# Performance work log

Hardware: AMD Instinct MI355X
Metric: run time of the kernel (lower is better)

## Reference

```python
import jax, jax.numpy as jnp
from jax import lax
import numpy as np

VOCAB, TAGS, EMB, HID = 50000, 45, 256, 512
B, S = 32, 256


def setup_inputs() -> dict:
    key = jax.random.key(0)
    ks = jax.random.split(key, 12)
    sc = 0.05
    return {
        "x": jax.random.randint(ks[0], (B, S), 0, VOCAB),
        "tags": jax.random.randint(ks[1], (B, S), 0, TAGS),
        "emb": jax.random.normal(ks[2], (VOCAB, EMB), jnp.float32) * sc,
        "w_ih_f": jax.random.normal(ks[3], (4 * HID, EMB), jnp.float32) * sc,
        "w_hh_f": jax.random.normal(ks[4], (4 * HID, HID), jnp.float32) * sc,
        "b_f": jnp.zeros((4 * HID,), jnp.float32),
        "w_ih_b": jax.random.normal(ks[5], (4 * HID, EMB), jnp.float32) * sc,
        "w_hh_b": jax.random.normal(ks[6], (4 * HID, HID), jnp.float32) * sc,
        "b_b": jnp.zeros((4 * HID,), jnp.float32),
        "lin_w": jax.random.normal(ks[7], (TAGS, 2 * HID), jnp.float32) * sc,
        "lin_b": jnp.zeros((TAGS,), jnp.float32),
        "start_t": jax.random.normal(ks[8], (TAGS,), jnp.float32) * 0.1,
        "end_t": jax.random.normal(ks[9], (TAGS,), jnp.float32) * 0.1,
        "trans": jax.random.normal(ks[10], (TAGS,), jnp.float32)[:, None] * 0.0 + jax.random.normal(ks[11], (TAGS, TAGS), jnp.float32) * 0.1,
    }


def _lstm_dir(xs, w_ih, w_hh, b, reverse):
    # xs: [B,S,E]. PyTorch gate order: i, f, g, o.
    Bsz = xs.shape[0]
    H = w_hh.shape[1]
    def step(carry, x_t):
        h, c = carry
        g = x_t @ w_ih.T + h @ w_hh.T + b
        i, f, gg, o = jnp.split(g, 4, axis=-1)
        c = jax.nn.sigmoid(f) * c + jax.nn.sigmoid(i) * jnp.tanh(gg)
        h = jax.nn.sigmoid(o) * jnp.tanh(c)
        return (h, c), h
    init = (jnp.zeros((Bsz, H), xs.dtype), jnp.zeros((Bsz, H), xs.dtype))
    _, hs = lax.scan(step, init, jnp.swapaxes(xs, 0, 1), reverse=reverse)
    return jnp.swapaxes(hs, 0, 1)  # [B,S,H]


def _crf_nll(em, tags, start_t, end_t, trans):
    # em: [B,S,T]; numerator: score of gold path
    em_sc = jnp.take_along_axis(em, tags[..., None], axis=2)[..., 0].sum(axis=1)
    tr_sc = trans[tags[:, :-1], tags[:, 1:]].sum(axis=1)
    score = start_t[tags[:, 0]] + em_sc + tr_sc + end_t[tags[:, -1]]
    # partition function via forward algorithm (logsumexp recurrence)
    alpha0 = start_t + em[:, 0]  # [B,T]
    def step(alpha, e_t):
        alpha = jax.nn.logsumexp(alpha[:, :, None] + trans[None], axis=1) + e_t
        return alpha, None
    alpha, _ = lax.scan(step, alpha0, jnp.swapaxes(em[:, 1:], 0, 1))
    logZ = jax.nn.logsumexp(alpha + end_t, axis=1)
    return -(score - logZ).mean()  # reduction='mean', loss = -llh


def reference(x, tags, emb, w_ih_f, w_hh_f, b_f, w_ih_b, w_hh_b, b_b,
              lin_w, lin_b, start_t, end_t, trans):
    embeds = emb[x]                               # [B,S,E]
    h_f = _lstm_dir(embeds, w_ih_f, w_hh_f, b_f, False)
    h_b = _lstm_dir(embeds, w_ih_b, w_hh_b, b_b, True)
    lstm_out = jnp.concatenate([h_f, h_b], axis=-1)  # [B,S,2H]
    emissions = lstm_out @ lin_w.T + lin_b           # [B,S,T]
    return _crf_nll(emissions, tags, start_t, end_t, trans)
```

## Files before the change

kernel.cpp:

```cpp
#include <hip/hip_runtime.h>

#define BB 32
#define SS 256
#define EMBD 256
#define HIDD 512
#define NTAG 45
#define TPAD 48
#define NBLK 32
#define APAD 520
#define GRID_REC 64
#define SENT 0x01010101u

typedef __bf16 bf16x8 __attribute__((ext_vector_type(8)));
typedef float  f32x4  __attribute__((ext_vector_type(4)));
typedef short  s16x8  __attribute__((ext_vector_type(8)));
typedef unsigned u32x4 __attribute__((ext_vector_type(4)));

__device__ __forceinline__ unsigned short f2bf(float x) {
  unsigned u = __builtin_bit_cast(unsigned, x);
  u = (u + 0x7fffu + ((u >> 16) & 1u)) >> 16;
  return (unsigned short)u;
}
__device__ __forceinline__ float bf2f(unsigned short u) {
  unsigned v = ((unsigned)u) << 16; return __builtin_bit_cast(float, v);
}

__device__ __forceinline__ void st32_sys(unsigned* p, unsigned v) {
  asm volatile("global_store_dword %0, %1, off sc0 sc1" :: "v"(p), "v"(v) : "memory");
}

#define LD8(CPOL)                                                           \
  asm volatile("global_load_dwordx4 %0, %[q0], off " CPOL "\n\t"            \
               "global_load_dwordx4 %1, %[q1], off " CPOL "\n\t"            \
               "global_load_dwordx4 %2, %[q2], off " CPOL "\n\t"            \
               "global_load_dwordx4 %3, %[q3], off " CPOL "\n\t"            \
               "global_load_dwordx4 %4, %[q4], off " CPOL "\n\t"            \
               "global_load_dwordx4 %5, %[q5], off " CPOL "\n\t"            \
               "global_load_dwordx4 %6, %[q6], off " CPOL "\n\t"            \
               "global_load_dwordx4 %7, %[q7], off " CPOL "\n\t"            \
               "s_waitcnt vmcnt(0)"                                         \
               : "=&v"(v0), "=&v"(v1), "=&v"(v2), "=&v"(v3),                \
                 "=&v"(v4), "=&v"(v5), "=&v"(v6), "=&v"(v7)                 \
               : [q0] "v"(p), [q1] "v"(p + 2048), [q2] "v"(p + 4096),       \
                 [q3] "v"(p + 6144), [q4] "v"(p + 8192), [q5] "v"(p + 10240),\
                 [q6] "v"(p + 12288), [q7] "v"(p + 14336)                   \
               : "memory")

__global__ void k_pack_e(const int* __restrict__ x, const float* __restrict__ emb,
                         unsigned short* __restrict__ E) {
  int idx = blockIdx.x * 256 + threadIdx.x;
  int e = idx & 255; int bt = idx >> 8; int b = bt & 31; int t = bt >> 5;
  int tok = x[b * SS + t];
  E[idx] = f2bf(emb[(long)tok * EMBD + e]);
}

__global__ void k_pack_w(const float* __restrict__ wih_f, const float* __restrict__ whh_f,
                         const float* __restrict__ bf_,  const float* __restrict__ wih_b,
                         const float* __restrict__ whh_b, const float* __restrict__ bb_,
                         unsigned short* __restrict__ Wh, unsigned short* __restrict__ Wie,
                         float* __restrict__ Bh) {
  long idx = (long)blockIdx.x * 256 + threadIdx.x;
  int k = (int)(idx % 768); long rest = idx / 768;
  int r2 = (int)(rest & 2047); int dir = (int)(rest >> 11);
  int blk = r2 >> 6, rl = r2 & 63, gate = rl >> 4, hl = rl & 15;
  int orig = gate * HIDD + blk * 16 + hl;
  const float* wih = dir ? wih_b : wih_f;
  const float* whh = dir ? whh_b : whh_f;
  if (k < HIDD) Wh[((long)(dir * 2048 + r2)) * 512 + k] = f2bf(whh[(long)orig * HIDD + k]);
  else          Wie[((long)(dir * 2048 + r2)) * 256 + (k - 512)] = f2bf(wih[(long)orig * EMBD + (k - 512)]);
  if (k == 0) {
    const float* bias = dir ? bb_ : bf_;
    Bh[dir * 2048 + r2] = bias[orig];
  }
}

__global__ void k_pack_l(const float* __restrict__ lin_w, const float* __restrict__ lin_b,
                         unsigned short* __restrict__ LW, float* __restrict__ LB) {
  int idx = blockIdx.x * 256 + threadIdx.x;
  if (idx < TPAD * 1024) {
    int tag = idx >> 10; int c = idx & 1023;
    LW[idx] = (tag < NTAG) ? f2bf(lin_w[tag * 1024 + c]) : (unsigned short)0;
  } else if (idx < TPAD * 1024 + TPAD) {
    int tag = idx - TPAD * 1024;
    LB[tag] = (tag < NTAG) ? lin_b[tag] : 0.f;
  }
}

__launch_bounds__(256)
__global__ void k_eproj(const unsigned short* __restrict__ E,
                        const unsigned short* __restrict__ Wie,
                        const float* __restrict__ Bh,
                        unsigned short* __restrict__ Ep) {
  __shared__ unsigned short W2[64 * 264];
  const int bx = blockIdx.x;
  const int tg = bx & 63, blk = (bx >> 6) & 31, dir = bx >> 11;
  const int tid = threadIdx.x;
  const int w = tid >> 6, lane = tid & 63;
  const int lm = lane & 15, quad = lane >> 4;

  {
    const unsigned short* src = Wie + ((long)(dir * 2048 + blk * 64)) * 256;
    for (int i = 0; i < 8; ++i) {
      int c = i * 256 + tid;
      int row = c >> 5, off = c & 31;
      *(s16x8*)&W2[row * 264 + off * 8] = *(const s16x8*)&src[row * 256 + off * 8];
    }
  }
  __syncthreads();

  f32x4 acc[2][4] = {};
#pragma unroll
  for (int kk = 0; kk < 8; ++kk) {
    s16x8 av[2];
#pragma unroll
    for (int sub = 0; sub < 2; ++sub)
      av[sub] = *(const s16x8*)&E[((long)(tg * 128 + w * 32 + sub * 16 + lm)) * 256 + kk * 32 + quad * 8];
#pragma unroll
    for (int sub = 0; sub < 2; ++sub)
#pragma unroll
      for (int n = 0; n < 4; ++n) {
        s16x8 bs = *(const s16x8*)&W2[(n * 16 + lm) * 264 + kk * 32 + quad * 8];
        acc[sub][n] = __builtin_amdgcn_mfma_f32_16x16x32_bf16(
            __builtin_bit_cast(bf16x8, av[sub]), __builtin_bit_cast(bf16x8, bs), acc[sub][n], 0, 0, 0);
      }
  }
  float bh[4];
#pragma unroll
  for (int n = 0; n < 4; ++n) bh[n] = Bh[dir * 2048 + blk * 64 + n * 16 + lm];
#pragma unroll
  for (int sub = 0; sub < 2; ++sub)
#pragma unroll
    for (int n = 0; n < 4; ++n)
#pragma unroll
      for (int r = 0; r < 4; ++r) {
        int m = w * 32 + sub * 16 + quad * 4 + r;
        int t = tg * 4 + (m >> 5), b = m & 31;
        int row_l = n * 16 + lm;
        Ep[((((long)(dir * 32 + blk) * 256 + t) * 32 + b) * 64) + row_l] =
            f2bf(acc[sub][n][r] + bh[n]);
      }
}

__launch_bounds__(256, 1)
__global__ void k_rec(const unsigned short* __restrict__ Wh,
                      const unsigned short* __restrict__ Ep,
                      unsigned short* __restrict__ H) {
  __shared__ unsigned short A_ls[32 * APAD];
  __shared__ float G_ls[32 * 66];

  const int bx = blockIdx.x;
  const int dir = bx & 1;
  const int blk = bx >> 1;
  const int tid = threadIdx.x;
  const int w = tid >> 6, lane = tid & 63;
  const int lm = lane & 15, quad = lane >> 4;
  const int mt = w >> 1, nt = w & 1;

  s16x8 wb[2][16];
  {
    const unsigned short* wsrc =
        Wh + ((long)(dir * 2048 + blk * 64 + nt * 32 + lm)) * 512 + quad * 8;
#pragma unroll
    for (int ns = 0; ns < 2; ++ns)
#pragma unroll
      for (int kk = 0; kk < 16; ++kk)
        wb[ns][kk] = *(const s16x8*)&wsrc[ns * 16 * 512 + kk * 32];
  }

  const int gb = tid >> 3, hp = tid & 7;
  float c0s = 0.f, c1s = 0.f;

  unsigned short* Hd = H + (long)dir * SS * BB * HIDD;
  const unsigned short* Epd = Ep + ((long)(dir * 32 + blk) * 256) * 32 * 64;

  for (int t = 0; t < SS; ++t) {
    const int tE = (dir == 0) ? t : (SS - 1 - t);

    unsigned short epv[8];
    {
      const unsigned short* eb =
          Epd + ((long)tE * 32 + (mt * 16 + quad * 4)) * 64 + nt * 32 + lm;
#pragma unroll
      for (int ns = 0; ns < 2; ++ns)
#pragma unroll
        for (int r = 0; r < 4; ++r) epv[ns * 4 + r] = eb[r * 64 + ns * 16];
    }

    f32x4 acc0 = {0.f, 0.f, 0.f, 0.f}, acc1 = {0.f, 0.f, 0.f, 0.f};
    if (t > 0) {
      {
        const int hslot = (dir == 0) ? (t - 1) : (SS - t);
        const unsigned short* p = Hd + (long)hslot * BB * HIDD + w * 512 + lane * 8;
        s16x8 v0, v1, v2, v3, v4, v5, v6, v7;
        unsigned bad;
        do {
          LD8("sc0 sc1");
          u32x4 u0 = __builtin_bit_cast(u32x4, v0), u1 = __builtin_bit_cast(u32x4, v1);
          u32x4 u2 = __builtin_bit_cast(u32x4, v2), u3 = __builtin_bit_cast(u32x4, v3);
          u32x4 u4 = __builtin_bit_cast(u32x4, v4), u5 = __builtin_bit_cast(u32x4, v5);
          u32x4 u6 = __builtin_bit_cast(u32x4, v6), u7 = __builtin_bit_cast(u32x4, v7);
          unsigned b0 = (u0.x == SENT) | (u0.y == SENT) | (u0.z == SENT) | (u0.w == SENT);
          unsigned b1 = (u1.x == SENT) | (u1.y == SENT) | (u1.z == SENT) | (u1.w == SENT);
          unsigned b2 = (u2.x == SENT) | (u2.y == SENT) | (u2.z == SENT) | (u2.w == SENT);
          unsigned b3 = (u3.x == SENT) | (u3.y == SENT) | (u3.z == SENT) | (u3.w == SENT);
          unsigned b4 = (u4.x == SENT) | (u4.y == SENT) | (u4.z == SENT) | (u4.w == SENT);
          unsigned b5 = (u5.x == SENT) | (u5.y == SENT) | (u5.z == SENT) | (u5.w == SENT);
          unsigned b6 = (u6.x == SENT) | (u6.y == SENT) | (u6.z == SENT) | (u6.w == SENT);
          unsigned b7 = (u7.x == SENT) | (u7.y == SENT) | (u7.z == SENT) | (u7.w == SENT);
          bad = (b0 | b1) | (b2 | b3) | ((b4 | b5) | (b6 | b7));
        } while (__builtin_expect(bad != 0u, 0));
        unsigned short* d = &A_ls[w * APAD + lane * 8];
        *(s16x8*)(d + 0 * 2080) = v0; *(s16x8*)(d + 1 * 2080) = v1;
        *(s16x8*)(d + 2 * 2080) = v2; *(s16x8*)(d + 3 * 2080) = v3;
        *(s16x8*)(d + 4 * 2080) = v4; *(s16x8*)(d + 5 * 2080) = v5;
        *(s16x8*)(d + 6 * 2080) = v6; *(s16x8*)(d + 7 * 2080) = v7;
      }
      __syncthreads();
#pragma unroll
      for (int kk = 0; kk < 16; ++kk) {
        s16x8 av = *(const s16x8*)&A_ls[(mt * 16 + lm) * APAD + kk * 32 + quad * 8];
        acc0 = __builtin_amdgcn_mfma_f32_16x16x32_bf16(
            __builtin_bit_cast(bf16x8, av), __builtin_bit_cast(bf16x8, wb[0][kk]), acc0, 0, 0, 0);
        acc1 = __builtin_amdgcn_mfma_f32_16x16x32_bf16(
            __builtin_bit_cast(bf16x8, av), __builtin_bit_cast(bf16x8, wb[1][kk]), acc1, 0, 0, 0);
      }
    }
#pragma unroll
    for (int r = 0; r < 4; ++r) {
      int mm = mt * 16 + quad * 4 + r;
      G_ls[mm * 66 + nt * 32 + lm]      = acc0[r] + bf2f(epv[r]);
      G_ls[mm * 66 + nt * 32 + 16 + lm] = acc1[r] + bf2f(epv[4 + r]);
    }
    __syncthreads();
    {
      float gi0 = G_ls[gb * 66 + 0  + 2 * hp], gi1 = G_ls[gb * 66 + 0  + 2 * hp + 1];
      float gf0 = G_ls[gb * 66 + 16 + 2 * hp], gf1 = G_ls[gb * 66 + 16 + 2 * hp + 1];
      float gg0 = G_ls[gb * 66 + 32 + 2 * hp], gg1 = G_ls[gb * 66 + 32 + 2 * hp + 1];
      float go0 = G_ls[gb * 66 + 48 + 2 * hp], go1 = G_ls[gb * 66 + 48 + 2 * hp + 1];
      float si0 = 1.f / (1.f + __expf(-gi0)), si1 = 1.f / (1.f + __expf(-gi1));
      float sf0 = 1.f / (1.f + __expf(-gf0)), sf1 = 1.f / (1.f + __expf(-gf1));
      float so0 = 1.f / (1.f + __expf(-go0)), so1 = 1.f / (1.f + __expf(-go1));
      float tg0 = tanhf(gg0), tg1 = tanhf(gg1);
      c0s = sf0 * c0s + si0 * tg0;
      c1s = sf1 * c1s + si1 * tg1;
      float h0 = so0 * tanhf(c0s), h1 = so1 * tanhf(c1s);
      int tslot = (dir == 0) ? t : (SS - 1 - t);
      unsigned hv = (unsigned)f2bf(h0) | ((unsigned)f2bf(h1) << 16);
      st32_sys((unsigned*)&Hd[(long)tslot * BB * HIDD + (long)gb * HIDD + blk * 16 + 2 * hp], hv);
    }
  }
}

__launch_bounds__(256)
__global__ void k_emis(const unsigned short* __restrict__ H,
                       const unsigned short* __restrict__ LW,
                       const float* __restrict__ LB,
                       float* __restrict__ EM) {
  const int row0 = blockIdx.x * 32;
  const int tid = threadIdx.x;
  const int w = tid >> 6, lane = tid & 63;
  const int lm = lane & 15, quad = lane >> 4;
  const unsigned short* Hf = H;
  const unsigned short* Hb = H + (long)SS * BB * HIDD;

  for (int tile = w; tile < 6; tile += 4) {
    int mt = tile / 3, nt = tile % 3;
    int arow = row0 + mt * 16 + lm;
    int nrow = nt * 16 + lm;
    f32x4 acc = {0.f, 0.f, 0.f, 0.f};
#pragma unroll 4
    for (int kk = 0; kk < 32; ++kk) {
      int k0 = kk * 32 + quad * 8;
      s16x8 asv = (k0 < HIDD) ? *(const s16x8*)&Hf[(long)arow * HIDD + k0]
                              : *(const s16x8*)&Hb[(long)arow * HIDD + (k0 - HIDD)];
      s16x8 bsv = *(const s16x8*)&LW[nrow * 1024 + k0];
      acc = __builtin_amdgcn_mfma_f32_16x16x32_bf16(
          __builtin_bit_cast(bf16x8, asv), __builtin_bit_cast(bf16x8, bsv), acc, 0, 0, 0);
    }
    float bias = LB[nrow];
#pragma unroll
    for (int r = 0; r < 4; ++r) {
      int mm = row0 + mt * 16 + quad * 4 + r;
      EM[(long)mm * TPAD + nrow] = acc[r] + bias;
    }
  }
}

__global__ void k_crf(const int* __restrict__ tags, const float* __restrict__ start_t,
                      const float* __restrict__ end_t, const float* __restrict__ trans,
                      const float* __restrict__ EM, float* __restrict__ chain) {
  __shared__ float T_ls[NTAG * TPAD];
  __shared__ float ET[48 * 48 + 16];
  __shared__ float P_ls[64];
  const int b = blockIdx.x;
  const int lane = threadIdx.x;
  const int j = lane;

  for (int i = lane; i < NTAG * NTAG; i += 64)
    T_ls[(i / NTAG) * TPAD + (i % NTAG)] = trans[i];
  for (int i = lane; i < 48 * 48 + 16; i += 64) ET[i] = 0.f;
  __syncthreads();

  float Mj = -1e30f;
  if (j < NTAG) {
    for (int i = 0; i < NTAG; ++i) Mj = fmaxf(Mj, T_ls[i * TPAD + j]);
    for (int i = 0; i < NTAG; ++i) ET[i * 48 + j] = __expf(T_ls[i * TPAD + j] - Mj);
  }
  __syncthreads();

  float et[48];
#pragma unroll
  for (int i = 0; i < 48; ++i) et[i] = ET[i * 48 + j];

  float part = 0.f;
  for (int t = lane; t < SS; t += 64) {
    int tg = tags[b * SS + t];
    part += EM[((long)t * BB + b) * TPAD + tg];
    if (t + 1 < SS) part += T_ls[tg * TPAD + tags[b * SS + t + 1]];
    if (t == 0)      part += start_t[tg];
    if (t == SS - 1) part += end_t[tg];
  }
  for (int off = 32; off; off >>= 1) part += __shfl_down(part, off);
  float score = __shfl(part, 0);

  float alpha = (j < NTAG) ? (start_t[j] + EM[(long)b * TPAD + j]) : -1e30f;
  float e_next = (j < NTAG) ? EM[((long)BB + b) * TPAD + j] : 0.f;
  for (int t = 1; t < SS; ++t) {
    float e_cur = e_next;
    if (t < SS - 1) e_next = (j < NTAG) ? EM[((long)(t + 1) * BB + b) * TPAD + j] : 0.f;
    float am = alpha;
#pragma unroll
    for (int off = 32; off; off >>= 1) am = fmaxf(am, __shfl_xor(am, off));
    float p = __expf(alpha - am);
    P_ls[lane] = p;
    __builtin_amdgcn_wave_barrier();
    float s0 = 0.f, s1 = 0.f, s2 = 0.f, s3 = 0.f;
#pragma unroll
    for (int i0 = 0; i0 < 48; i0 += 4) {
      f32x4 pv = *(const f32x4*)&P_ls[i0];
      s0 += pv.x * et[i0];
      s1 += pv.y * et[i0 + 1];
      s2 += pv.z * et[i0 + 2];
      s3 += pv.w * et[i0 + 3];
    }
    __builtin_amdgcn_wave_barrier();
    float s = (s0 + s1) + (s2 + s3);
    float na = am + Mj + __logf(s) + e_cur;
    alpha = (j < NTAG) ? na : -1e30f;
  }
  float v = (j < NTAG) ? (alpha + end_t[j]) : -1e30f;
  float mx = v;
  for (int off = 32; off; off >>= 1) mx = fmaxf(mx, __shfl_xor(mx, off));
  float s = __expf(v - mx);
  for (int off = 32; off; off >>= 1) s += __shfl_xor(s, off);
  if (lane == 0) chain[b] = score - (mx + __logf(s));
}

__global__ void k_fin(const float* __restrict__ chain, float* __restrict__ out) {
  int lane = threadIdx.x;
  float v = (lane < BB) ? chain[lane] : 0.f;
  for (int off = 32; off; off >>= 1) v += __shfl_xor(v, off);
  if (lane == 0) out[0] = -v / (float)BB;
}

extern "C" void kernel_launch(void* const* d_in, const int* in_sizes, int n_in,
                              void* d_out, int out_size, void* d_ws, size_t ws_size,
                              hipStream_t stream) {
  const int*   x      = (const int*)d_in[0];
  const int*   tags   = (const int*)d_in[1];
  const float* emb    = (const float*)d_in[2];
  const float* wih_f  = (const float*)d_in[3];
  const float* whh_f  = (const float*)d_in[4];
  const float* b_f    = (const float*)d_in[5];
  const float* wih_b  = (const float*)d_in[6];
  const float* whh_b  = (const float*)d_in[7];
  const float* b_b    = (const float*)d_in[8];
  const float* lin_w  = (const float*)d_in[9];
  const float* lin_b  = (const float*)d_in[10];
  const float* start_t= (const float*)d_in[11];
  const float* end_t  = (const float*)d_in[12];
  const float* trans  = (const float*)d_in[13];

  char* ws = (char*)d_ws;
  size_t off = 0;
  auto alloc = [&](size_t bytes) {
    void* p = ws + off; off = (off + bytes + 255) & ~(size_t)255; return p;
  };
  unsigned short* E   = (unsigned short*)alloc((size_t)SS * BB * EMBD * 2);
  unsigned short* Wh  = (unsigned short*)alloc((size_t)2 * 2048 * 512 * 2);
  unsigned short* Wie = (unsigned short*)alloc((size_t)2 * 2048 * 256 * 2);
  float*          Bh  = (float*)         alloc((size_t)2 * 2048 * 4);
  unsigned short* Ep  = (unsigned short*)alloc((size_t)2 * 32 * 256 * 32 * 64 * 2);
  unsigned short* H   = (unsigned short*)alloc((size_t)2 * SS * BB * HIDD * 2);
  unsigned short* LW  = (unsigned short*)alloc((size_t)TPAD * 1024 * 2);
  float*          LB  = (float*)         alloc((size_t)TPAD * 4);
  float*          EM  = (float*)         alloc((size_t)SS * BB * TPAD * 4);
  float*          chain = (float*)       alloc((size_t)BB * 4);

  hipMemsetAsync(H, 0x01, (size_t)2 * SS * BB * HIDD * 2, stream);
  k_pack_e<<<dim3((SS * BB * EMBD) / 256), dim3(256), 0, stream>>>(x, emb, E);
  k_pack_w<<<dim3((2 * 2048 * 768) / 256), dim3(256), 0, stream>>>(
      wih_f, whh_f, b_f, wih_b, whh_b, b_b, Wh, Wie, Bh);
  k_pack_l<<<dim3((TPAD * 1024 + TPAD + 255) / 256), dim3(256), 0, stream>>>(
      lin_w, lin_b, LW, LB);
  k_eproj<<<dim3(4096), dim3(256), 0, stream>>>(E, Wie, Bh, Ep);

  void* kargs[] = {&Wh, &Ep, &H};
  hipLaunchCooperativeKernel((const void*)k_rec, dim3(GRID_REC), dim3(256), kargs, 0, stream);

  k_emis<<<dim3((SS * BB) / 32), dim3(256), 0, stream>>>(H, LW, LB, EM);
  k_crf<<<dim3(BB), dim3(64), 0, stream>>>(tags, start_t, end_t, trans, EM, chain);
  k_fin<<<dim3(1), dim3(64), 0, stream>>>(chain, (float*)d_out);
}
```

Baseline: 1.105 ms.

## Halve recurrent grid so each block owns 32 hidden units; use fast activations

The recurrent LSTM kernel now runs on half as many blocks (16 per direction instead of 32). Each block covers 128 gate rows (32 hidden units), and each wave computes a 32x32 output tile with four MFMAs per k-step. This halves the number of blocks that must synchronise through global memory at every timestep and widens the hidden-state stores to 64-bit system-scope writes. The sigmoid and tanh use hardware exp2/rcp approximations in place of __expf and tanhf, trading a little accuracy. Each block now does twice the per-step compute and the grid occupies fewer CUs, which may lengthen the serial per-step critical path.

```diff
diff --git a/kernel.cpp b/kernel.cpp
--- a/kernel.cpp
+++ b/kernel.cpp
@@ -6,9 +6,10 @@
 #define HIDD 512
 #define NTAG 45
 #define TPAD 48
-#define NBLK 32
+#define NBLK 16
 #define APAD 520
-#define GRID_REC 64
+#define GRID_REC 32
+#define GSTR 130
 #define SENT 0x01010101u
 
 typedef __bf16 bf16x8 __attribute__((ext_vector_type(8)));
@@ -24,9 +25,18 @@
 __device__ __forceinline__ float bf2f(unsigned short u) {
   unsigned v = ((unsigned)u) << 16; return __builtin_bit_cast(float, v);
 }
-
-__device__ __forceinline__ void st32_sys(unsigned* p, unsigned v) {
-  asm volatile("global_store_dword %0, %1, off sc0 sc1" :: "v"(p), "v"(v) : "memory");
+__device__ __forceinline__ float fsig(float x) {
+  float e = __builtin_amdgcn_exp2f(-1.44269504f * x);
+  return __builtin_amdgcn_rcpf(1.f + e);
+}
+__device__ __forceinline__ float ftanh(float x) {
+  float e = __builtin_amdgcn_exp2f(-2.88539008f * x);
+  return 2.f * __builtin_amdgcn_rcpf(1.f + e) - 1.f;
+}
+
+__device__ __forceinline__ void st64_sys(unsigned* p, unsigned a, unsigned b) {
+  unsigned long long v = ((unsigned long long)b << 32) | (unsigned long long)a;
+  asm volatile("global_store_dwordx2 %0, %1, off sc0 sc1" :: "v"(p), "v"(v) : "memory");
 }
 
 #define LD8(CPOL)                                                           \
@@ -146,7 +156,7 @@
                       const unsigned short* __restrict__ Ep,
                       unsigned short* __restrict__ H) {
   __shared__ unsigned short A_ls[32 * APAD];
-  __shared__ float G_ls[32 * 66];
+  __shared__ float G_ls[32 * GSTR];
 
   const int bx = blockIdx.x;
   const int dir = bx & 1;
@@ -154,12 +164,11 @@
   const int tid = threadIdx.x;
   const int w = tid >> 6, lane = tid & 63;
   const int lm = lane & 15, quad = lane >> 4;
-  const int mt = w >> 1, nt = w & 1;
 
   s16x8 wb[2][16];
   {
     const unsigned short* wsrc =
-        Wh + ((long)(dir * 2048 + blk * 64 + nt * 32 + lm)) * 512 + quad * 8;
+        Wh + ((long)(dir * 2048 + blk * 128 + w * 32 + lm)) * 512 + quad * 8;
 #pragma unroll
     for (int ns = 0; ns < 2; ++ns)
 #pragma unroll
@@ -167,26 +176,30 @@
         wb[ns][kk] = *(const s16x8*)&wsrc[ns * 16 * 512 + kk * 32];
   }
 
-  const int gb = tid >> 3, hp = tid & 7;
-  float c0s = 0.f, c1s = 0.f;
+  const int m_act = tid >> 3, cg = tid & 7;
+  float cst[4] = {0.f, 0.f, 0.f, 0.f};
 
   unsigned short* Hd = H + (long)dir * SS * BB * HIDD;
-  const unsigned short* Epd = Ep + ((long)(dir * 32 + blk) * 256) * 32 * 64;
+  const unsigned short* Epw =
+      Ep + ((long)(dir * 32 + 2 * blk + (w >> 1)) * 256) * 32 * 64;
+  const int ep_col = (w & 1) * 32 + lm;
 
   for (int t = 0; t < SS; ++t) {
     const int tE = (dir == 0) ? t : (SS - 1 - t);
 
-    unsigned short epv[8];
+    unsigned short epv[16];
     {
-      const unsigned short* eb =
-          Epd + ((long)tE * 32 + (mt * 16 + quad * 4)) * 64 + nt * 32 + lm;
-#pragma unroll
-      for (int ns = 0; ns < 2; ++ns)
-#pragma unroll
-        for (int r = 0; r < 4; ++r) epv[ns * 4 + r] = eb[r * 64 + ns * 16];
-    }
-
-    f32x4 acc0 = {0.f, 0.f, 0.f, 0.f}, acc1 = {0.f, 0.f, 0.f, 0.f};
+      const unsigned short* eb = Epw + ((long)tE * 32 + quad * 4) * 64 + ep_col;
+#pragma unroll
+      for (int mt = 0; mt < 2; ++mt)
+#pragma unroll
+        for (int ns = 0; ns < 2; ++ns)
+#pragma unroll
+          for (int r = 0; r < 4; ++r)
+            epv[mt * 8 + ns * 4 + r] = eb[(mt * 16 + r) * 64 + ns * 16];
+    }
+
+    f32x4 acc[2][2] = {};
     if (t > 0) {
       {
         const int hslot = (dir == 0) ? (t - 1) : (SS - t);
@@ -218,35 +231,47 @@
       __syncthreads();
 #pragma unroll
       for (int kk = 0; kk < 16; ++kk) {
-        s16x8 av = *(const s16x8*)&A_ls[(mt * 16 + lm) * APAD + kk * 32 + quad * 8];
-        acc0 = __builtin_amdgcn_mfma_f32_16x16x32_bf16(
-            __builtin_bit_cast(bf16x8, av), __builtin_bit_cast(bf16x8, wb[0][kk]), acc0, 0, 0, 0);
-        acc1 = __builtin_amdgcn_mfma_f32_16x16x32_bf16(
-            __builtin_bit_cast(bf16x8, av), __builtin_bit_cast(bf16x8, wb[1][kk]), acc1, 0, 0, 0);
+        s16x8 av0 = *(const s16x8*)&A_ls[(lm)      * APAD + kk * 32 + quad * 8];
+        s16x8 av1 = *(const s16x8*)&A_ls[(16 + lm) * APAD + kk * 32 + quad * 8];
+        acc[0][0] = __builtin_amdgcn_mfma_f32_16x16x32_bf16(
+            __builtin_bit_cast(bf16x8, av0), __builtin_bit_cast(bf16x8, wb[0][kk]), acc[0][0], 0, 0, 0);
+        acc[0][1] = __builtin_amdgcn_mfma_f32_16x16x32_bf16(
+            __builtin_bit_cast(bf16x8, av0), __builtin_bit_cast(bf16x8, wb[1][kk]), acc[0][1], 0, 0, 0);
+        acc[1][0] = __builtin_amdgcn_mfma_f32_16x16x32_bf16(
+            __builtin_bit_cast(bf16x8, av1), __builtin_bit_cast(bf16x8, wb[0][kk]), acc[1][0], 0, 0, 0);
+        acc[1][1] = __builtin_amdgcn_mfma_f32_16x16x32_bf16(
+            __builtin_bit_cast(bf16x8, av1), __builtin_bit_cast(bf16x8, wb[1][kk]), acc[1][1], 0, 0, 0);
       }
     }
 #pragma unroll
-    for (int r = 0; r < 4; ++r) {
-      int mm = mt * 16 + quad * 4 + r;
-      G_ls[mm * 66 + nt * 32 + lm]      = acc0[r] + bf2f(epv[r]);
-      G_ls[mm * 66 + nt * 32 + 16 + lm] = acc1[r] + bf2f(epv[4 + r]);
-    }
+    for (int mt = 0; mt < 2; ++mt)
+#pragma unroll
+      for (int ns = 0; ns < 2; ++ns)
+#pragma unroll
+        for (int r = 0; r < 4; ++r) {
+          int mm = mt * 16 + quad * 4 + r;
+          G_ls[mm * GSTR + w * 32 + ns * 16 + lm] =
+              acc[mt][ns][r] + bf2f(epv[mt * 8 + ns * 4 + r]);
+        }
     __syncthreads();
     {
-      float gi0 = G_ls[gb * 66 + 0  + 2 * hp], gi1 = G_ls[gb * 66 + 0  + 2 * hp + 1];
-      float gf0 = G_ls[gb * 66 + 16 + 2 * hp], gf1 = G_ls[gb * 66 + 16 + 2 * hp + 1];
-      float gg0 = G_ls[gb * 66 + 32 + 2 * hp], gg1 = G_ls[gb * 66 + 32 + 2 * hp + 1];
-      float go0 = G_ls[gb * 66 + 48 + 2 * hp], go1 = G_ls[gb * 66 + 48 + 2 * hp + 1];
-      float si0 = 1.f / (1.f + __expf(-gi0)), si1 = 1.f / (1.f + __expf(-gi1));
-      float sf0 = 1.f / (1.f + __expf(-gf0)), sf1 = 1.f / (1.f + __expf(-gf1));
-      float so0 = 1.f / (1.f + __expf(-go0)), so1 = 1.f / (1.f + __expf(-go1));
-      float tg0 = tanhf(gg0), tg1 = tanhf(gg1);
-      c0s = sf0 * c0s + si0 * tg0;
-      c1s = sf1 * c1s + si1 * tg1;
-      float h0 = so0 * tanhf(c0s), h1 = so1 * tanhf(c1s);
+      float hv[4];
+#pragma unroll
+      for (int j = 0; j < 4; ++j) {
+        int c = cg * 4 + j, sub = c >> 4, hl = c & 15;
+        const float* gp = &G_ls[m_act * GSTR + sub * 64 + hl];
+        float si = fsig(gp[0]);
+        float sf = fsig(gp[16]);
+        float tg = ftanh(gp[32]);
+        float so = fsig(gp[48]);
+        cst[j] = sf * cst[j] + si * tg;
+        hv[j] = so * ftanh(cst[j]);
+      }
       int tslot = (dir == 0) ? t : (SS - 1 - t);
-      unsigned hv = (unsigned)f2bf(h0) | ((unsigned)f2bf(h1) << 16);
-      st32_sys((unsigned*)&Hd[(long)tslot * BB * HIDD + (long)gb * HIDD + blk * 16 + 2 * hp], hv);
+      unsigned d0 = (unsigned)f2bf(hv[0]) | ((unsigned)f2bf(hv[1]) << 16);
+      unsigned d1 = (unsigned)f2bf(hv[2]) | ((unsigned)f2bf(hv[3]) << 16);
+      st64_sys((unsigned*)&Hd[(long)tslot * BB * HIDD + (long)m_act * HIDD + blk * 32 + cg * 4],
+               d0, d1);
     }
   }
 }
```

Result: faster. 1.083 ms (-2.0%).
